# Kernel optimization log

Measured on AMD Instinct MI355X. Metric: run time of the kernel, lower is better.

The kernel has to match this reference:

```python
import jax, jax.numpy as jnp
import numpy as np

# Model dims (match init_kwargs)
E = 2048   # embed_dim
H = 16     # num_heads
QR = 512   # q_low_rank
KVR = 512  # kv_low_rank
DR = 64    # rope_dim
DV = 128   # v_head_dim
S = 2048   # seq_len


def _make_rotary(seq_len, dim):
    inv_freq = 1.0 / jnp.power(10000.0, jnp.arange(0, dim, 2, dtype=jnp.float32) / dim)
    t = jnp.arange(seq_len, dtype=jnp.float32)
    freqs = jnp.outer(t, inv_freq)  # (S, dim//2)
    return jnp.sin(freqs), jnp.cos(freqs)


def _apply_rope(x, sin, cos):
    # x: (S, H_or_1, D); sin/cos: (S, D//2)
    d = x.shape[-1] // 2
    x1, x2 = x[..., :d], x[..., d:]
    s = jnp.concatenate([sin, sin], axis=-1)[:, None, :]
    c = jnp.concatenate([cos, cos], axis=-1)[:, None, :]
    return x * c + jnp.concatenate([-x2, x1], axis=-1) * s


def setup_inputs() -> dict:
    key = jax.random.key(0)
    ks = jax.random.split(key, 8)
    def lin(k, out_dim, in_dim):
        return jax.random.normal(k, (out_dim, in_dim), dtype=jnp.float32) * (1.0 / np.sqrt(in_dim))
    return {
        "x": jax.random.normal(ks[0], (S, E), dtype=jnp.float32),
        "wq_down": lin(ks[1], QR, E),
        "wq_up": lin(ks[2], H * DV, QR),
        "wq_rope": lin(ks[3], H * DR, QR),
        "wkv_down": lin(ks[4], KVR, E),
        "wkv_up": lin(ks[5], H * 2 * DV, KVR),
        "wk_rope": lin(ks[6], DR, E),
        "wo": lin(ks[7], E, H * DV),
    }


def reference(x, wq_down, wq_up, wq_rope, wkv_down, wkv_up, wk_rope, wo):
    seq = x.shape[0]
    # Query path: low-rank bottleneck -> content + rope streams
    c_q = x @ wq_down.T                                   # (S, QR)
    q_content = (c_q @ wq_up.T).reshape(seq, H, DV)       # (S, H, DV)
    q_rope = (c_q @ wq_rope.T).reshape(seq, H, DR)        # (S, H, DR)
    # KV path: shared low-rank bottleneck
    c_kv = x @ wkv_down.T                                 # (S, KVR)
    kv = c_kv @ wkv_up.T                                  # (S, 2*H*DV)
    k_content_flat, v_flat = jnp.split(kv, 2, axis=-1)
    k_content = k_content_flat.reshape(seq, H, DV)
    v = v_flat.reshape(seq, H, DV)
    # Shared key-RoPE projection (one per position, broadcast over heads)
    k_rope_shared = (x @ wk_rope.T)[:, None, :]           # (S, 1, DR)
    sin, cos = _make_rotary(seq, DR)
    q_rope_rot = _apply_rope(q_rope, sin, cos)            # (S, H, DR)
    k_rope_rot = _apply_rope(k_rope_shared, sin, cos)     # (S, 1, DR)
    # Concat content + rope streams; QK head dim = DV + DR
    dt = jnp.bfloat16
    q = jnp.concatenate([q_content, q_rope_rot], axis=-1).astype(dt)                            # (S, H, DV+DR)
    k = jnp.concatenate([k_content, jnp.broadcast_to(k_rope_rot, (seq, H, DR))], axis=-1).astype(dt)
    v_attn = v.astype(dt)
    scale = 1.0 / np.sqrt(DV + DR)
    # Attention. Note: original zero-pads V to DV+DR then slices output back to
    # DV -- mathematically identical to attending with unpadded V.
    logits = jnp.einsum('shd,thd->hst', q, k).astype(jnp.float32) * scale  # (H, S, S)
    probs = jax.nn.softmax(logits, axis=-1).astype(dt)
    attn = jnp.einsum('hst,thd->shd', probs, v_attn)      # (S, H, DV)
    attn_flat = attn.reshape(seq, H * DV)
    return (attn_flat @ wo.T).astype(jnp.float32)         # (S, E)
```

## Files before the change

### kernel.cpp

```cpp
#include <hip/hip_runtime.h>
#include <stdint.h>
#include <math.h>

#define S_LEN 2048
#define NH 16

typedef __attribute__((ext_vector_type(8))) short bf16x8;
typedef __attribute__((ext_vector_type(4))) float f32x4;
typedef __attribute__((ext_vector_type(16))) float f32x16;
typedef unsigned short ush;

__device__ __forceinline__ ush f2bf(float f) {
  union { float f; unsigned u; } v; v.f = f;
  unsigned x = v.u;
  return (ush)((x + 0x7fffu + ((x >> 16) & 1u)) >> 16);
}
__device__ __forceinline__ float bf2f(ush b) {
  union { unsigned u; float f; } v; v.u = ((unsigned)b) << 16;
  return v.f;
}
__device__ __forceinline__ ush f2h(float f) {
  _Float16 h = (_Float16)f;
  union { _Float16 h; ush u; } v; v.h = h;
  return v.u;
}
__device__ __forceinline__ float h2f(ush u) {
  union { ush u; _Float16 h; } v; v.u = u;
  return (float)v.h;
}

__device__ __forceinline__ void gload_lds16(const ush* g, ush* l) {
  __builtin_amdgcn_global_load_lds((const __attribute__((address_space(1))) void*)g,
                                   (__attribute__((address_space(3))) void*)l, 16, 0, 0);
}

__global__ void mega_pack(const float* __restrict__ wq_down, const float* __restrict__ wkv_down,
                          const float* __restrict__ wk_rope, const float* __restrict__ wq_up,
                          const float* __restrict__ wq_rope, const float* __restrict__ wkv_up,
                          const float* __restrict__ wo, const float* __restrict__ x,
                          ush* __restrict__ wdh, ush* __restrict__ wqh, ush* __restrict__ wkvuh,
                          ush* __restrict__ woh, ush* __restrict__ xh, float* __restrict__ tab) {
  int idx = blockIdx.x * 256 + threadIdx.x;
  if (idx < 2359296) {
    int r = idx >> 11, c = idx & 2047;
    float v = (r < 512) ? wq_down[(size_t)r * 2048 + c]
            : (r < 1024) ? wkv_down[(size_t)(r - 512) * 2048 + c]
            : (r < 1088) ? wk_rope[(size_t)(r - 1024) * 2048 + c] : 0.f;
    wdh[idx] = f2h(v);
    return;
  }
  idx -= 2359296;
  if (idx < 1572864) {
    int r = idx >> 9, c = idx & 511;
    float v = (r < 2048) ? wq_up[(size_t)r * 512 + c] : wq_rope[(size_t)(r - 2048) * 512 + c];
    wqh[idx] = f2h(v);
    return;
  }
  idx -= 1572864;
  if (idx < 2097152) { wkvuh[idx] = f2h(wkv_up[idx]); return; }
  idx -= 2097152;
  if (idx < 4194304) { woh[idx] = f2h(wo[idx]); return; }
  idx -= 4194304;
  if (idx < 4194304) { xh[idx] = f2h(x[idx]); return; }
  idx -= 4194304;
  if (idx < 65536) {
    int tt = idx >> 5, i = idx & 31;
    float inv_freq = 1.0f / powf(10000.0f, (float)i * (1.0f / 32.0f));
    float fr = (float)tt * inv_freq;
    tab[idx] = sinf(fr);
    tab[65536 + idx] = cosf(fr);
  }
}

__global__ __launch_bounds__(256) void gemm_down(
    const ush* __restrict__ A, const ush* __restrict__ B,
    ush* __restrict__ cqh, ush* __restrict__ ckvh, float* __restrict__ krl) {
  constexpr int K = 2048;
  __shared__ __align__(16) ush As[64 * 32];
  __shared__ __align__(16) ush Bs[64 * 32];
  const int t = threadIdx.x, l = t & 63, w = t >> 6;
  const int wm = w & 1, wn = w >> 1;
  const int m0 = blockIdx.y * 64, n0 = blockIdx.x * 64;
  const int lm = l & 15, lq = l >> 4;
  const int lr = l >> 2, lc = (l & 3) * 8;

  f32x4 acc[2][2];
  const f32x4 zero = {0.f, 0.f, 0.f, 0.f};
#pragma unroll
  for (int i = 0; i < 2; i++)
#pragma unroll
    for (int j = 0; j < 2; j++) acc[i][j] = zero;

  const ush* Ag = A + (size_t)(m0 + w * 16 + lr) * K + lc;
  const ush* Bg = B + (size_t)(n0 + w * 16 + lr) * K + lc;
  ush* Al = As + w * 512;
  ush* Bl = Bs + w * 512;

  for (int k0 = 0; k0 < K; k0 += 32) {
    __syncthreads();
    gload_lds16(Ag + k0, Al);
    gload_lds16(Bg + k0, Bl);
    __syncthreads();
    bf16x8 af[2], bfr[2];
#pragma unroll
    for (int i = 0; i < 2; i++)
      af[i] = *(const bf16x8*)(As + (wm * 32 + i * 16 + lm) * 32 + lq * 8);
#pragma unroll
    for (int j = 0; j < 2; j++)
      bfr[j] = *(const bf16x8*)(Bs + (wn * 32 + j * 16 + lm) * 32 + lq * 8);
#pragma unroll
    for (int i = 0; i < 2; i++)
#pragma unroll
      for (int j = 0; j < 2; j++)
        acc[i][j] = __builtin_amdgcn_mfma_f32_16x16x32_f16(af[i], bfr[j], acc[i][j], 0, 0, 0);
  }

#pragma unroll
  for (int i = 0; i < 2; i++)
#pragma unroll
    for (int j = 0; j < 2; j++)
#pragma unroll
      for (int r = 0; r < 4; r++) {
        int mm = m0 + wm * 32 + i * 16 + lq * 4 + r;
        int nn = n0 + wn * 32 + j * 16 + lm;
        float v = acc[i][j][r];
        if (nn < 512)       cqh[(size_t)mm * 512 + nn] = f2h(v);
        else if (nn < 1024) ckvh[(size_t)mm * 512 + nn - 512] = f2h(v);
        else if (nn < 1088) krl[(size_t)mm * 64 + nn - 1024] = v;
      }
}

__global__ __launch_bounds__(256) void gemm_up(
    const ush* __restrict__ cqh, const ush* __restrict__ wqh,
    const ush* __restrict__ ckvh, const ush* __restrict__ wkvuh,
    ush* __restrict__ qupf, ush* __restrict__ kvf) {
  constexpr int BM = 128, BN = 64, K = 512, FI = 4, FJ = 2;
  __shared__ __align__(16) ush As[BM * 32];
  __shared__ __align__(16) ush Bs[BN * 32];
  int bx = blockIdx.x;
  const ush* A; const ush* B; ush* C; int ldc;
  if (bx < 48) { A = cqh; B = wqh; C = qupf; ldc = 3072; }
  else { bx -= 48; A = ckvh; B = wkvuh; C = kvf; ldc = 4096; }
  const int t = threadIdx.x, l = t & 63, w = t >> 6;
  const int wm = w & 1, wn = w >> 1;
  const int m0 = blockIdx.y * BM, n0 = bx * BN;
  const int lm = l & 15, lq = l >> 4;
  const int lr = l >> 2, lc = (l & 3) * 8;

  f32x4 acc[FI][FJ];
  const f32x4 zero = {0.f, 0.f, 0.f, 0.f};
#pragma unroll
  for (int i = 0; i < FI; i++)
#pragma unroll
    for (int j = 0; j < FJ; j++) acc[i][j] = zero;

  const ush* Ag[2];
#pragma unroll
  for (int i = 0; i < 2; i++) Ag[i] = A + (size_t)(m0 + w * 32 + i * 16 + lr) * K + lc;
  const ush* Bg = B + (size_t)(n0 + w * 16 + lr) * K + lc;
  ush* Al = As + w * (BM * 8);
  ush* Bl = Bs + w * (BN * 8);

  for (int k0 = 0; k0 < K; k0 += 32) {
    __syncthreads();
#pragma unroll
    for (int i = 0; i < 2; i++) gload_lds16(Ag[i] + k0, Al + i * 512);
    gload_lds16(Bg + k0, Bl);
    __syncthreads();
    bf16x8 af[FI], bfr[FJ];
#pragma unroll
    for (int i = 0; i < FI; i++)
      af[i] = *(const bf16x8*)(As + (wm * 64 + i * 16 + lm) * 32 + lq * 8);
#pragma unroll
    for (int j = 0; j < FJ; j++)
      bfr[j] = *(const bf16x8*)(Bs + (wn * 32 + j * 16 + lm) * 32 + lq * 8);
#pragma unroll
    for (int i = 0; i < FI; i++)
#pragma unroll
      for (int j = 0; j < FJ; j++)
        acc[i][j] = __builtin_amdgcn_mfma_f32_16x16x32_f16(af[i], bfr[j], acc[i][j], 0, 0, 0);
  }

#pragma unroll
  for (int i = 0; i < FI; i++)
#pragma unroll
    for (int j = 0; j < FJ; j++)
#pragma unroll
      for (int r = 0; r < 4; r++) {
        int mm = m0 + wm * 64 + i * 16 + lq * 4 + r;
        int nn = n0 + wn * 32 + j * 16 + lm;
        C[(size_t)mm * ldc + nn] = f2h(acc[i][j][r]);
      }
}

__global__ __launch_bounds__(256) void gemm_out(
    const ush* __restrict__ A, const ush* __restrict__ B, float* __restrict__ C,
    int K, int ldc) {
  constexpr int BM = 128, BN = 64, FI = 4, FJ = 2;
  __shared__ __align__(16) ush As[BM * 32];
  __shared__ __align__(16) ush Bs[BN * 32];
  const int t = threadIdx.x, l = t & 63, w = t >> 6;
  const int wm = w & 1, wn = w >> 1;
  const int m0 = blockIdx.y * BM, n0 = blockIdx.x * BN;
  const int lm = l & 15, lq = l >> 4;
  const int lr = l >> 2, lc = (l & 3) * 8;

  f32x4 acc[FI][FJ];
  const f32x4 zero = {0.f, 0.f, 0.f, 0.f};
#pragma unroll
  for (int i = 0; i < FI; i++)
#pragma unroll
    for (int j = 0; j < FJ; j++) acc[i][j] = zero;

  const ush* Ag[2];
#pragma unroll
  for (int i = 0; i < 2; i++) Ag[i] = A + (size_t)(m0 + w * 32 + i * 16 + lr) * K + lc;
  const ush* Bg = B + (size_t)(n0 + w * 16 + lr) * K + lc;
  ush* Al = As + w * (BM * 8);
  ush* Bl = Bs + w * (BN * 8);

  for (int k0 = 0; k0 < K; k0 += 32) {
    __syncthreads();
#pragma unroll
    for (int i = 0; i < 2; i++) gload_lds16(Ag[i] + k0, Al + i * 512);
    gload_lds16(Bg + k0, Bl);
    __syncthreads();
    bf16x8 af[FI], bfr[FJ];
#pragma unroll
    for (int i = 0; i < FI; i++)
      af[i] = *(const bf16x8*)(As + (wm * 64 + i * 16 + lm) * 32 + lq * 8);
#pragma unroll
    for (int j = 0; j < FJ; j++)
      bfr[j] = *(const bf16x8*)(Bs + (wn * 32 + j * 16 + lm) * 32 + lq * 8);
#pragma unroll
    for (int i = 0; i < FI; i++)
#pragma unroll
      for (int j = 0; j < FJ; j++)
        acc[i][j] = __builtin_amdgcn_mfma_f32_16x16x32_f16(af[i], bfr[j], acc[i][j], 0, 0, 0);
  }

#pragma unroll
  for (int i = 0; i < FI; i++)
#pragma unroll
    for (int j = 0; j < FJ; j++)
#pragma unroll
      for (int r = 0; r < 4; r++) {
        int mm = m0 + wm * 64 + i * 16 + lq * 4 + r;
        int nn = n0 + wn * 32 + j * 16 + lm;
        C[(size_t)mm * ldc + nn] = acc[i][j][r];
      }
}

__global__ void build_all(const ush* __restrict__ qupf, const ush* __restrict__ kvf,
                          const float* __restrict__ krl, const float* __restrict__ tab,
                          ush* __restrict__ qb, ush* __restrict__ kbt, ush* __restrict__ vtt) {
  const float scale = 0.07216878364870323f;
  if (blockIdx.x >= 50176) {
    __shared__ ush Vt[128 * 72];
    int b = blockIdx.x - 50176;
    const int T = b & 31, h = b >> 5, t = threadIdx.x;
    const int key = t >> 5, d0 = (t & 31) * 4;
#pragma unroll
    for (int pass = 0; pass < 8; ++pass) {
      int k = key + pass * 8;
      int s = T * 64 + k;
      ushort4 v = *(const ushort4*)(kvf + (size_t)s * 4096 + 2048 + h * 128 + d0);
      Vt[(d0 + 0) * 72 + k] = f2bf(h2f(v.x));
      Vt[(d0 + 1) * 72 + k] = f2bf(h2f(v.y));
      Vt[(d0 + 2) * 72 + k] = f2bf(h2f(v.z));
      Vt[(d0 + 3) * 72 + k] = f2bf(h2f(v.w));
    }
    __syncthreads();
    ush* dst = vtt + (size_t)(h * 32 + T) * 9216;
    for (int off = t; off < 1152; off += 256) {
      int row = off / 9, c8 = (off % 9) * 8;
      *(bf16x8*)(dst + row * 72 + c8) = *(const bf16x8*)(Vt + row * 72 + c8);
    }
    return;
  }
  int idx = blockIdx.x * 256 + threadIdx.x;
  if (idx < 6291456) {
    int d = idx % 192; int sh = idx / 192; int h = sh & 15; int s = sh >> 4;
    ush v;
    if (d < 128) {
      v = f2bf(h2f(qupf[(size_t)s * 3072 + h * 128 + d]) * scale);
    } else {
      int r = d - 128, i = r & 31;
      float sn = tab[s * 32 + i], cs = tab[65536 + s * 32 + i];
      const ush* qr = qupf + (size_t)s * 3072 + 2048 + h * 64;
      float xv = h2f(qr[r]);
      float other = (r < 32) ? -h2f(qr[r + 32]) : h2f(qr[r - 32]);
      v = f2bf((xv * cs + other * sn) * scale);
    }
    qb[((size_t)h * S_LEN + s) * 192 + d] = v;
    return;
  }
  idx -= 6291456;
  if (idx < 6553600) {
    int c = idx % 200; int r2 = idx / 200;
    int key = r2 & 63; int r3 = r2 >> 6; int T = r3 & 31; int h = r3 >> 5;
    int s = T * 64 + key;
    ush v = 0;
    if (c < 128) {
      v = f2bf(h2f(kvf[(size_t)s * 4096 + h * 128 + c]));
    } else if (c < 192) {
      int r = c - 128, i = r & 31;
      float sn = tab[s * 32 + i], cs = tab[65536 + s * 32 + i];
      const float* kr = krl + (size_t)s * 64;
      float xv = kr[r];
      float other = (r < 32) ? -kr[r + 32] : kr[r - 32];
      v = f2bf(xv * cs + other * sn);
    }
    kbt[((size_t)(h * 32 + T) * 64 + key) * 200 + c] = v;
  }
}

__global__ __launch_bounds__(512, 2) void attn_fused(
    const ush* __restrict__ qb, const ush* __restrict__ kbt, const ush* __restrict__ vtt,
    ush* __restrict__ opart, float* __restrict__ ml) {
  __shared__ __align__(16) ush Ks[2][64 * 200];
  __shared__ __align__(16) ush Vs[2][128 * 72];
  const int t = threadIdx.x, l = t & 63, w = t >> 6;
  const int id = blockIdx.x + 8 * (blockIdx.y + 16 * blockIdx.z);
  const int wid = (id & 7) * 32 + (id >> 3);
  const int qx = wid & 7, h = (wid >> 3) & 15, z = wid >> 7;
  const int qrow0 = qx * 256 + w * 32;
  const int ln = l & 31, lh = l >> 5;

  bf16x8 qf[12];
#pragma unroll
  for (int st = 0; st < 12; st++)
    qf[st] = *(const bf16x8*)(qb + ((size_t)h * S_LEN + qrow0 + ln) * 192 + st * 16 + lh * 8);
#pragma unroll
  for (int st = 0; st < 12; st++) asm volatile("" : "+v"(qf[st]));

  f32x16 o[4];
#pragma unroll
  for (int i = 0; i < 4; i++)
#pragma unroll
    for (int r = 0; r < 16; r++) o[i][r] = 0.f;
  float ps = 0.f;

  const ush* kbase = kbt + (size_t)(h * 32 + z * 16) * 12800;
  const ush* vbase = vtt + (size_t)(h * 32 + z * 16) * 9216;

  for (int c = w; c < 43; c += 8) {
    if (c < 25) gload_lds16(kbase + c * 512 + l * 8, &Ks[0][c * 512]);
    else        gload_lds16(vbase + (c - 25) * 512 + l * 8, &Vs[0][(c - 25) * 512]);
  }
  asm volatile("s_waitcnt vmcnt(0)" ::: "memory");
  __builtin_amdgcn_s_barrier();
  __builtin_amdgcn_sched_barrier(0);

  int cur = 0;
  for (int it = 0; it < 16; ++it) {
    if (it < 15) {
      const ush* ksrc = kbase + (size_t)(it + 1) * 12800;
      const ush* vsrc = vbase + (size_t)(it + 1) * 9216;
      ush* kd = &Ks[cur ^ 1][0];
      ush* vd = &Vs[cur ^ 1][0];
      for (int c = w; c < 43; c += 8) {
        if (c < 25) gload_lds16(ksrc + c * 512 + l * 8, kd + c * 512);
        else        gload_lds16(vsrc + (c - 25) * 512 + l * 8, vd + (c - 25) * 512);
      }
      __builtin_amdgcn_sched_barrier(0);
      asm volatile("s_waitcnt vmcnt(5)" ::: "memory");
    } else {
      asm volatile("s_waitcnt vmcnt(0)" ::: "memory");
    }
    __builtin_amdgcn_s_barrier();
    __builtin_amdgcn_sched_barrier(0);

    const ush* Kb = &Ks[cur][0];
    const ush* Vb = &Vs[cur][0];

    f32x16 sv[2];
#pragma unroll
    for (int kb = 0; kb < 2; kb++)
#pragma unroll
      for (int r = 0; r < 16; r++) sv[kb][r] = 0.f;

    __builtin_amdgcn_s_setprio(1);
#pragma unroll
    for (int kb = 0; kb < 2; kb++)
#pragma unroll
      for (int st = 0; st < 12; st++) {
        bf16x8 af = *(const bf16x8*)(Kb + (kb * 32 + ln) * 200 + st * 16 + lh * 8);
        sv[kb] = __builtin_amdgcn_mfma_f32_32x32x16_bf16(af, qf[st], sv[kb], 0, 0, 0);
      }
    __builtin_amdgcn_s_setprio(0);

#pragma unroll
    for (int kb = 0; kb < 2; kb++) {
      unsigned pk8[8];
#pragma unroll
      for (int g = 0; g < 4; g++) {
        float p0 = __expf(sv[kb][4 * g + 0]);
        float p1 = __expf(sv[kb][4 * g + 1]);
        float p2 = __expf(sv[kb][4 * g + 2]);
        float p3 = __expf(sv[kb][4 * g + 3]);
        ps += (p0 + p1) + (p2 + p3);
        unsigned lo, hi;
        asm("v_cvt_pk_bf16_f32 %0, %1, %2" : "=v"(lo) : "v"(p0), "v"(p1));
        asm("v_cvt_pk_bf16_f32 %0, %1, %2" : "=v"(hi) : "v"(p2), "v"(p3));
        pk8[2 * g] = lo; pk8[2 * g + 1] = hi;
      }
      asm("v_permlane32_swap_b32 %0, %1" : "+v"(pk8[0]), "+v"(pk8[2]));
      asm("v_permlane32_swap_b32 %0, %1" : "+v"(pk8[1]), "+v"(pk8[3]));
      asm("v_permlane32_swap_b32 %0, %1" : "+v"(pk8[4]), "+v"(pk8[6]));
      asm("v_permlane32_swap_b32 %0, %1" : "+v"(pk8[5]), "+v"(pk8[7]));
      union { unsigned d[4]; bf16x8 v; } pf0u, pf1u;
      pf0u.d[0] = pk8[0]; pf0u.d[1] = pk8[1]; pf0u.d[2] = pk8[2]; pf0u.d[3] = pk8[3];
      pf1u.d[0] = pk8[4]; pf1u.d[1] = pk8[5]; pf1u.d[2] = pk8[6]; pf1u.d[3] = pk8[7];

      __builtin_amdgcn_s_setprio(1);
#pragma unroll
      for (int db = 0; db < 4; db++) {
        bf16x8 vf0 = *(const bf16x8*)(Vb + (db * 32 + ln) * 72 + kb * 32 + lh * 8);
        bf16x8 vf1 = *(const bf16x8*)(Vb + (db * 32 + ln) * 72 + kb * 32 + 16 + lh * 8);
        o[db] = __builtin_amdgcn_mfma_f32_32x32x16_bf16(vf0, pf0u.v, o[db], 0, 0, 0);
        o[db] = __builtin_amdgcn_mfma_f32_32x32x16_bf16(vf1, pf1u.v, o[db], 0, 0, 0);
      }
      __builtin_amdgcn_s_setprio(0);
    }

    __builtin_amdgcn_s_barrier();
    __builtin_amdgcn_sched_barrier(0);
    cur ^= 1;
  }

  float lsum = ps + __shfl_xor(ps, 32, 64);
  const int s = qrow0 + ln;
  const size_t rbase = ((size_t)((z * 16 + h) * 2048) + s) * 128;
#pragma unroll
  for (int db = 0; db < 4; db++)
#pragma unroll
    for (int rq = 0; rq < 4; rq++) {
      ushort4 v4;
      v4.x = f2h(o[db][rq * 4 + 0] * 0.0625f);
      v4.y = f2h(o[db][rq * 4 + 1] * 0.0625f);
      v4.z = f2h(o[db][rq * 4 + 2] * 0.0625f);
      v4.w = f2h(o[db][rq * 4 + 3] * 0.0625f);
      *(ushort4*)(&opart[rbase + db * 32 + 8 * rq + 4 * lh]) = v4;
    }
  if (lh == 0) ml[(size_t)(z * 16 + h) * 2048 + s] = lsum;
}

__global__ __launch_bounds__(256) void attn_reduce(const ush* __restrict__ opart,
                                                   const float* __restrict__ ml,
                                                   ush* __restrict__ attnh) {
  int row = blockIdx.x * 4 + (threadIdx.x >> 6);
  int l = threadIdx.x & 63;
  int h = row >> 11, s = row & 2047;
  float lsum = 0.f;
#pragma unroll
  for (int z = 0; z < 2; z++) lsum += ml[(size_t)(z * 16 + h) * 2048 + s];
  float inv = 16.0f / lsum;
#pragma unroll
  for (int c0 = 0; c0 < 128; c0 += 64) {
    int c = c0 + l;
    float acc = 0.f;
#pragma unroll
    for (int z = 0; z < 2; z++)
      acc += h2f(opart[((size_t)(z * 16 + h) * 2048 + s) * 128 + c]);
    attnh[(size_t)s * 2048 + h * 128 + c] = f2h(bf2f(f2bf(acc * inv)));
  }
}

extern "C" void kernel_launch(void* const* d_in, const int* in_sizes, int n_in,
                              void* d_out, int out_size, void* d_ws, size_t ws_size,
                              hipStream_t stream) {
  const float* x        = (const float*)d_in[0];
  const float* wq_down  = (const float*)d_in[1];
  const float* wq_up    = (const float*)d_in[2];
  const float* wq_rope  = (const float*)d_in[3];
  const float* wkv_down = (const float*)d_in[4];
  const float* wkv_up   = (const float*)d_in[5];
  const float* wk_rope  = (const float*)d_in[6];
  const float* wo       = (const float*)d_in[7];
  char* ws = (char*)d_ws;

  size_t off = 0;
  auto alloc = [&](size_t b) { size_t c = off; off += (b + 255) & ~(size_t)255; return c; };
  const size_t XH    = alloc(2048UL * 2048 * 2);
  const size_t WDH   = alloc(1152UL * 2048 * 2);
  const size_t KRL   = alloc(2048UL * 64 * 4);
  const size_t CQH   = alloc(2048UL * 512 * 2);
  const size_t CKVH  = alloc(2048UL * 512 * 2);
  const size_t WQH   = alloc(3072UL * 512 * 2);
  const size_t QUPF  = alloc(2048UL * 3072 * 2);
  const size_t WKVUH = alloc(4096UL * 512 * 2);
  const size_t WOH   = alloc(2048UL * 2048 * 2);
  const size_t KVF   = alloc(2048UL * 4096 * 2);
  const size_t QB    = alloc(16UL * 2048 * 192 * 2);
  const size_t KBT   = alloc(16UL * 32 * 12800 * 2);
  const size_t VTT   = alloc(16UL * 32 * 9216 * 2);
  const size_t TAB   = alloc(2048UL * 32 * 4 * 2);
  const size_t OPART = alloc(2UL * 16 * 2048 * 128 * 2);
  const size_t ML    = alloc(2UL * 16 * 2048 * 4);
  const size_t ATTNH = XH;

  mega_pack<<<dim3(56576), 256, 0, stream>>>(
      wq_down, wkv_down, wk_rope, wq_up, wq_rope, wkv_up, wo, x,
      (ush*)(ws + WDH), (ush*)(ws + WQH), (ush*)(ws + WKVUH),
      (ush*)(ws + WOH), (ush*)(ws + XH), (float*)(ws + TAB));

  gemm_down<<<dim3(18, 32), 256, 0, stream>>>(
      (ush*)(ws + XH), (ush*)(ws + WDH),
      (ush*)(ws + CQH), (ush*)(ws + CKVH), (float*)(ws + KRL));

  gemm_up<<<dim3(112, 16), 256, 0, stream>>>(
      (ush*)(ws + CQH), (ush*)(ws + WQH),
      (ush*)(ws + CKVH), (ush*)(ws + WKVUH),
      (ush*)(ws + QUPF), (ush*)(ws + KVF));

  build_all<<<dim3(50688), 256, 0, stream>>>(
      (const ush*)(ws + QUPF), (const ush*)(ws + KVF), (const float*)(ws + KRL),
      (const float*)(ws + TAB), (ush*)(ws + QB), (ush*)(ws + KBT), (ush*)(ws + VTT));

  attn_fused<<<dim3(8, 16, 2), 512, 0, stream>>>(
      (ush*)(ws + QB), (ush*)(ws + KBT), (ush*)(ws + VTT),
      (ush*)(ws + OPART), (float*)(ws + ML));
  attn_reduce<<<dim3(8192), 256, 0, stream>>>((const ush*)(ws + OPART), (const float*)(ws + ML),
                                              (ush*)(ws + ATTNH));

  gemm_out<<<dim3(32, 16), 256, 0, stream>>>(
      (ush*)(ws + ATTNH), (ush*)(ws + WOH), (float*)d_out, 2048, 2048);
}
```

Baseline: 311.6 us.

## Double-buffer LDS in GEMMs and interleave softmax with MFMA in attention

The three GEMM kernels (down, up, out) now use double-buffered LDS tiles, prefetching the next K-slice while MFMAs run on the current one, with one barrier per iteration instead of two. The attention loop moves its wait and barrier to the top of each iteration. It then reorders the two 32-key sub-blocks so the exp/pack of the first overlaps the QK MFMAs of the second and the PV MFMAs of the first. Costs are doubled LDS in the GEMMs, possibly lower occupancy, and higher register pressure. The attention prefetch now waits with vmcnt(0) at the start of the next iteration rather than a partial wait.

New measurement: 303.5 us. 1.03x faster.

```diff
diff --git a/kernel.cpp b/kernel.cpp
--- a/kernel.cpp
+++ b/kernel.cpp
@@ -76,8 +76,8 @@
     const ush* __restrict__ A, const ush* __restrict__ B,
     ush* __restrict__ cqh, ush* __restrict__ ckvh, float* __restrict__ krl) {
   constexpr int K = 2048;
-  __shared__ __align__(16) ush As[64 * 32];
-  __shared__ __align__(16) ush Bs[64 * 32];
+  __shared__ __align__(16) ush As[2 * 64 * 32];
+  __shared__ __align__(16) ush Bs[2 * 64 * 32];
   const int t = threadIdx.x, l = t & 63, w = t >> 6;
   const int wm = w & 1, wn = w >> 1;
   const int m0 = blockIdx.y * 64, n0 = blockIdx.x * 64;
@@ -93,26 +93,36 @@
 
   const ush* Ag = A + (size_t)(m0 + w * 16 + lr) * K + lc;
   const ush* Bg = B + (size_t)(n0 + w * 16 + lr) * K + lc;
-  ush* Al = As + w * 512;
-  ush* Bl = Bs + w * 512;
-
+
+  gload_lds16(Ag, As + w * 512);
+  gload_lds16(Bg, Bs + w * 512);
+
+  int cur = 0;
   for (int k0 = 0; k0 < K; k0 += 32) {
-    __syncthreads();
-    gload_lds16(Ag + k0, Al);
-    gload_lds16(Bg + k0, Bl);
-    __syncthreads();
+    asm volatile("s_waitcnt vmcnt(0)" ::: "memory");
+    __builtin_amdgcn_s_barrier();
+    __builtin_amdgcn_sched_barrier(0);
+    if (k0 + 32 < K) {
+      int nb = cur ^ 1;
+      gload_lds16(Ag + k0 + 32, As + nb * 2048 + w * 512);
+      gload_lds16(Bg + k0 + 32, Bs + nb * 2048 + w * 512);
+    }
+    __builtin_amdgcn_sched_barrier(0);
+    const ush* Asc = As + cur * 2048;
+    const ush* Bsc = Bs + cur * 2048;
     bf16x8 af[2], bfr[2];
 #pragma unroll
     for (int i = 0; i < 2; i++)
-      af[i] = *(const bf16x8*)(As + (wm * 32 + i * 16 + lm) * 32 + lq * 8);
+      af[i] = *(const bf16x8*)(Asc + (wm * 32 + i * 16 + lm) * 32 + lq * 8);
 #pragma unroll
     for (int j = 0; j < 2; j++)
-      bfr[j] = *(const bf16x8*)(Bs + (wn * 32 + j * 16 + lm) * 32 + lq * 8);
+      bfr[j] = *(const bf16x8*)(Bsc + (wn * 32 + j * 16 + lm) * 32 + lq * 8);
 #pragma unroll
     for (int i = 0; i < 2; i++)
 #pragma unroll
       for (int j = 0; j < 2; j++)
         acc[i][j] = __builtin_amdgcn_mfma_f32_16x16x32_f16(af[i], bfr[j], acc[i][j], 0, 0, 0);
+    cur ^= 1;
   }
 
 #pragma unroll
@@ -135,8 +145,8 @@
     const ush* __restrict__ ckvh, const ush* __restrict__ wkvuh,
     ush* __restrict__ qupf, ush* __restrict__ kvf) {
   constexpr int BM = 128, BN = 64, K = 512, FI = 4, FJ = 2;
-  __shared__ __align__(16) ush As[BM * 32];
-  __shared__ __align__(16) ush Bs[BN * 32];
+  __shared__ __align__(16) ush As[2 * BM * 32];
+  __shared__ __align__(16) ush Bs[2 * BN * 32];
   int bx = blockIdx.x;
   const ush* A; const ush* B; ush* C; int ldc;
   if (bx < 48) { A = cqh; B = wqh; C = qupf; ldc = 3072; }
@@ -158,27 +168,39 @@
 #pragma unroll
   for (int i = 0; i < 2; i++) Ag[i] = A + (size_t)(m0 + w * 32 + i * 16 + lr) * K + lc;
   const ush* Bg = B + (size_t)(n0 + w * 16 + lr) * K + lc;
-  ush* Al = As + w * (BM * 8);
-  ush* Bl = Bs + w * (BN * 8);
-
+
+#pragma unroll
+  for (int i = 0; i < 2; i++) gload_lds16(Ag[i], As + w * 1024 + i * 512);
+  gload_lds16(Bg, Bs + w * 512);
+
+  int cur = 0;
   for (int k0 = 0; k0 < K; k0 += 32) {
-    __syncthreads();
-#pragma unroll
-    for (int i = 0; i < 2; i++) gload_lds16(Ag[i] + k0, Al + i * 512);
-    gload_lds16(Bg + k0, Bl);
-    __syncthreads();
+    asm volatile("s_waitcnt vmcnt(0)" ::: "memory");
+    __builtin_amdgcn_s_barrier();
+    __builtin_amdgcn_sched_barrier(0);
+    if (k0 + 32 < K) {
+      int nb = cur ^ 1;
+#pragma unroll
+      for (int i = 0; i < 2; i++)
+        gload_lds16(Ag[i] + k0 + 32, As + nb * 4096 + w * 1024 + i * 512);
+      gload_lds16(Bg + k0 + 32, Bs + nb * 2048 + w * 512);
+    }
+    __builtin_amdgcn_sched_barrier(0);
+    const ush* Asc = As + cur * 4096;
+    const ush* Bsc = Bs + cur * 2048;
     bf16x8 af[FI], bfr[FJ];
 #pragma unroll
     for (int i = 0; i < FI; i++)
-      af[i] = *(const bf16x8*)(As + (wm * 64 + i * 16 + lm) * 32 + lq * 8);
+      af[i] = *(const bf16x8*)(Asc + (wm * 64 + i * 16 + lm) * 32 + lq * 8);
 #pragma unroll
     for (int j = 0; j < FJ; j++)
-      bfr[j] = *(const bf16x8*)(Bs + (wn * 32 + j * 16 + lm) * 32 + lq * 8);
+      bfr[j] = *(const bf16x8*)(Bsc + (wn * 32 + j * 16 + lm) * 32 + lq * 8);
 #pragma unroll
     for (int i = 0; i < FI; i++)
 #pragma unroll
       for (int j = 0; j < FJ; j++)
         acc[i][j] = __builtin_amdgcn_mfma_f32_16x16x32_f16(af[i], bfr[j], acc[i][j], 0, 0, 0);
+    cur ^= 1;
   }
 
 #pragma unroll
@@ -197,8 +219,8 @@
     const ush* __restrict__ A, const ush* __restrict__ B, float* __restrict__ C,
     int K, int ldc) {
   constexpr int BM = 128, BN = 64, FI = 4, FJ = 2;
-  __shared__ __align__(16) ush As[BM * 32];
-  __shared__ __align__(16) ush Bs[BN * 32];
+  __shared__ __align__(16) ush As[2 * BM * 32];
+  __shared__ __align__(16) ush Bs[2 * BN * 32];
   const int t = threadIdx.x, l = t & 63, w = t >> 6;
   const int wm = w & 1, wn = w >> 1;
   const int m0 = blockIdx.y * BM, n0 = blockIdx.x * BN;
@@ -216,27 +238,39 @@
 #pragma unroll
   for (int i = 0; i < 2; i++) Ag[i] = A + (size_t)(m0 + w * 32 + i * 16 + lr) * K + lc;
   const ush* Bg = B + (size_t)(n0 + w * 16 + lr) * K + lc;
-  ush* Al = As + w * (BM * 8);
-  ush* Bl = Bs + w * (BN * 8);
-
+
+#pragma unroll
+  for (int i = 0; i < 2; i++) gload_lds16(Ag[i], As + w * 1024 + i * 512);
+  gload_lds16(Bg, Bs + w * 512);
+
+  int cur = 0;
   for (int k0 = 0; k0 < K; k0 += 32) {
-    __syncthreads();
-#pragma unroll
-    for (int i = 0; i < 2; i++) gload_lds16(Ag[i] + k0, Al + i * 512);
-    gload_lds16(Bg + k0, Bl);
-    __syncthreads();
+    asm volatile("s_waitcnt vmcnt(0)" ::: "memory");
+    __builtin_amdgcn_s_barrier();
+    __builtin_amdgcn_sched_barrier(0);
+    if (k0 + 32 < K) {
+      int nb = cur ^ 1;
+#pragma unroll
+      for (int i = 0; i < 2; i++)
+        gload_lds16(Ag[i] + k0 + 32, As + nb * 4096 + w * 1024 + i * 512);
+      gload_lds16(Bg + k0 + 32, Bs + nb * 2048 + w * 512);
+    }
+    __builtin_amdgcn_sched_barrier(0);
+    const ush* Asc = As + cur * 4096;
+    const ush* Bsc = Bs + cur * 2048;
     bf16x8 af[FI], bfr[FJ];
 #pragma unroll
     for (int i = 0; i < FI; i++)
-      af[i] = *(const bf16x8*)(As + (wm * 64 + i * 16 + lm) * 32 + lq * 8);
+      af[i] = *(const bf16x8*)(Asc + (wm * 64 + i * 16 + lm) * 32 + lq * 8);
 #pragma unroll
     for (int j = 0; j < FJ; j++)
-      bfr[j] = *(const bf16x8*)(Bs + (wn * 32 + j * 16 + lm) * 32 + lq * 8);
+      bfr[j] = *(const bf16x8*)(Bsc + (wn * 32 + j * 16 + lm) * 32 + lq * 8);
 #pragma unroll
     for (int i = 0; i < FI; i++)
 #pragma unroll
       for (int j = 0; j < FJ; j++)
         acc[i][j] = __builtin_amdgcn_mfma_f32_16x16x32_f16(af[i], bfr[j], acc[i][j], 0, 0, 0);
+    cur ^= 1;
   }
 
 #pragma unroll
@@ -344,16 +378,40 @@
   const ush* kbase = kbt + (size_t)(h * 32 + z * 16) * 12800;
   const ush* vbase = vtt + (size_t)(h * 32 + z * 16) * 9216;
 
+  auto smpack = [&ps](const f32x16& svv, bf16x8& f0, bf16x8& f1) {
+    unsigned pk8[8];
+#pragma unroll
+    for (int g = 0; g < 4; g++) {
+      float p0 = __expf(svv[4 * g + 0]);
+      float p1 = __expf(svv[4 * g + 1]);
+      float p2 = __expf(svv[4 * g + 2]);
+      float p3 = __expf(svv[4 * g + 3]);
+      ps += (p0 + p1) + (p2 + p3);
+      unsigned lo, hi;
+      asm("v_cvt_pk_bf16_f32 %0, %1, %2" : "=v"(lo) : "v"(p0), "v"(p1));
+      asm("v_cvt_pk_bf16_f32 %0, %1, %2" : "=v"(hi) : "v"(p2), "v"(p3));
+      pk8[2 * g] = lo; pk8[2 * g + 1] = hi;
+    }
+    asm("v_permlane32_swap_b32 %0, %1" : "+v"(pk8[0]), "+v"(pk8[2]));
+    asm("v_permlane32_swap_b32 %0, %1" : "+v"(pk8[1]), "+v"(pk8[3]));
+    asm("v_permlane32_swap_b32 %0, %1" : "+v"(pk8[4]), "+v"(pk8[6]));
+    asm("v_permlane32_swap_b32 %0, %1" : "+v"(pk8[5]), "+v"(pk8[7]));
+    union { unsigned d[4]; bf16x8 v; } u0, u1;
+    u0.d[0] = pk8[0]; u0.d[1] = pk8[1]; u0.d[2] = pk8[2]; u0.d[3] = pk8[3];
+    u1.d[0] = pk8[4]; u1.d[1] = pk8[5]; u1.d[2] = pk8[6]; u1.d[3] = pk8[7];
+    f0 = u0.v; f1 = u1.v;
+  };
+
   for (int c = w; c < 43; c += 8) {
     if (c < 25) gload_lds16(kbase + c * 512 + l * 8, &Ks[0][c * 512]);
     else        gload_lds16(vbase + (c - 25) * 512 + l * 8, &Vs[0][(c - 25) * 512]);
   }
-  asm volatile("s_waitcnt vmcnt(0)" ::: "memory");
-  __builtin_amdgcn_s_barrier();
-  __builtin_amdgcn_sched_barrier(0);
 
   int cur = 0;
   for (int it = 0; it < 16; ++it) {
+    asm volatile("s_waitcnt vmcnt(0)" ::: "memory");
+    __builtin_amdgcn_s_barrier();
+    __builtin_amdgcn_sched_barrier(0);
     if (it < 15) {
       const ush* ksrc = kbase + (size_t)(it + 1) * 12800;
       const ush* vsrc = vbase + (size_t)(it + 1) * 9216;
@@ -363,69 +421,58 @@
         if (c < 25) gload_lds16(ksrc + c * 512 + l * 8, kd + c * 512);
         else        gload_lds16(vsrc + (c - 25) * 512 + l * 8, vd + (c - 25) * 512);
       }
-      __builtin_amdgcn_sched_barrier(0);
-      asm volatile("s_waitcnt vmcnt(5)" ::: "memory");
-    } else {
-      asm volatile("s_waitcnt vmcnt(0)" ::: "memory");
-    }
-    __builtin_amdgcn_s_barrier();
+    }
     __builtin_amdgcn_sched_barrier(0);
 
     const ush* Kb = &Ks[cur][0];
     const ush* Vb = &Vs[cur][0];
 
-    f32x16 sv[2];
-#pragma unroll
-    for (int kb = 0; kb < 2; kb++)
-#pragma unroll
-      for (int r = 0; r < 16; r++) sv[kb][r] = 0.f;
+    f32x16 sv0, sv1;
+#pragma unroll
+    for (int r = 0; r < 16; r++) { sv0[r] = 0.f; sv1[r] = 0.f; }
 
     __builtin_amdgcn_s_setprio(1);
 #pragma unroll
-    for (int kb = 0; kb < 2; kb++)
-#pragma unroll
-      for (int st = 0; st < 12; st++) {
-        bf16x8 af = *(const bf16x8*)(Kb + (kb * 32 + ln) * 200 + st * 16 + lh * 8);
-        sv[kb] = __builtin_amdgcn_mfma_f32_32x32x16_bf16(af, qf[st], sv[kb], 0, 0, 0);
-      }
+    for (int st = 0; st < 12; st++) {
+      bf16x8 af = *(const bf16x8*)(Kb + ln * 200 + st * 16 + lh * 8);
+      sv0 = __builtin_amdgcn_mfma_f32_32x32x16_bf16(af, qf[st], sv0, 0, 0, 0);
+    }
     __builtin_amdgcn_s_setprio(0);
 
-#pragma unroll
-    for (int kb = 0; kb < 2; kb++) {
-      unsigned pk8[8];
-#pragma unroll
-      for (int g = 0; g < 4; g++) {
-        float p0 = __expf(sv[kb][4 * g + 0]);
-        float p1 = __expf(sv[kb][4 * g + 1]);
-        float p2 = __expf(sv[kb][4 * g + 2]);
-        float p3 = __expf(sv[kb][4 * g + 3]);
-        ps += (p0 + p1) + (p2 + p3);
-        unsigned lo, hi;
-        asm("v_cvt_pk_bf16_f32 %0, %1, %2" : "=v"(lo) : "v"(p0), "v"(p1));
-        asm("v_cvt_pk_bf16_f32 %0, %1, %2" : "=v"(hi) : "v"(p2), "v"(p3));
-        pk8[2 * g] = lo; pk8[2 * g + 1] = hi;
-      }
-      asm("v_permlane32_swap_b32 %0, %1" : "+v"(pk8[0]), "+v"(pk8[2]));
-      asm("v_permlane32_swap_b32 %0, %1" : "+v"(pk8[1]), "+v"(pk8[3]));
-      asm("v_permlane32_swap_b32 %0, %1" : "+v"(pk8[4]), "+v"(pk8[6]));
-      asm("v_permlane32_swap_b32 %0, %1" : "+v"(pk8[5]), "+v"(pk8[7]));
-      union { unsigned d[4]; bf16x8 v; } pf0u, pf1u;
-      pf0u.d[0] = pk8[0]; pf0u.d[1] = pk8[1]; pf0u.d[2] = pk8[2]; pf0u.d[3] = pk8[3];
-      pf1u.d[0] = pk8[4]; pf1u.d[1] = pk8[5]; pf1u.d[2] = pk8[6]; pf1u.d[3] = pk8[7];
-
-      __builtin_amdgcn_s_setprio(1);
-#pragma unroll
-      for (int db = 0; db < 4; db++) {
-        bf16x8 vf0 = *(const bf16x8*)(Vb + (db * 32 + ln) * 72 + kb * 32 + lh * 8);
-        bf16x8 vf1 = *(const bf16x8*)(Vb + (db * 32 + ln) * 72 + kb * 32 + 16 + lh * 8);
-        o[db] = __builtin_amdgcn_mfma_f32_32x32x16_bf16(vf0, pf0u.v, o[db], 0, 0, 0);
-        o[db] = __builtin_amdgcn_mfma_f32_32x32x16_bf16(vf1, pf1u.v, o[db], 0, 0, 0);
-      }
-      __builtin_amdgcn_s_setprio(0);
-    }
-
-    __builtin_amdgcn_s_barrier();
-    __builtin_amdgcn_sched_barrier(0);
+    bf16x8 pf00, pf01;
+    smpack(sv0, pf00, pf01);
+
+    __builtin_amdgcn_s_setprio(1);
+#pragma unroll
+    for (int st = 0; st < 12; st++) {
+      bf16x8 af = *(const bf16x8*)(Kb + (32 + ln) * 200 + st * 16 + lh * 8);
+      sv1 = __builtin_amdgcn_mfma_f32_32x32x16_bf16(af, qf[st], sv1, 0, 0, 0);
+    }
+    __builtin_amdgcn_s_setprio(0);
+
+    __builtin_amdgcn_s_setprio(1);
+#pragma unroll
+    for (int db = 0; db < 4; db++) {
+      bf16x8 vf0 = *(const bf16x8*)(Vb + (db * 32 + ln) * 72 + lh * 8);
+      bf16x8 vf1 = *(const bf16x8*)(Vb + (db * 32 + ln) * 72 + 16 + lh * 8);
+      o[db] = __builtin_amdgcn_mfma_f32_32x32x16_bf16(vf0, pf00, o[db], 0, 0, 0);
+      o[db] = __builtin_amdgcn_mfma_f32_32x32x16_bf16(vf1, pf01, o[db], 0, 0, 0);
+    }
+    __builtin_amdgcn_s_setprio(0);
+
+    bf16x8 pf10, pf11;
+    smpack(sv1, pf10, pf11);
+
+    __builtin_amdgcn_s_setprio(1);
+#pragma unroll
+    for (int db = 0; db < 4; db++) {
+      bf16x8 vf0 = *(const bf16x8*)(Vb + (db * 32 + ln) * 72 + 32 + lh * 8);
+      bf16x8 vf1 = *(const bf16x8*)(Vb + (db * 32 + ln) * 72 + 48 + lh * 8);
+      o[db] = __builtin_amdgcn_mfma_f32_32x32x16_bf16(vf0, pf10, o[db], 0, 0, 0);
+      o[db] = __builtin_amdgcn_mfma_f32_32x32x16_bf16(vf1, pf11, o[db], 0, 0, 0);
+    }
+    __builtin_amdgcn_s_setprio(0);
+
     cur ^= 1;
   }
 
```
